# Kernel optimization log

Hardware: AMD Instinct MI355X
Metric: run time of the kernel (lower is better)

The kernel has to match this reference:

```python
import jax, jax.numpy as jnp
import numpy as np
import math

B, N, DMODEL, H = 8, 1024, 256, 8
HEAD_DIM = DMODEL // H


def setup_inputs() -> dict:
    key = jax.random.key(0)
    ks = jax.random.split(key, 8)
    x = jax.random.normal(ks[0], (B, N, DMODEL), dtype=jnp.float32)
    # symmetric-ish nonnegative pairwise distances
    adj = jax.random.uniform(ks[1], (B, N, N), dtype=jnp.float32) * 10.0
    mask = jax.random.uniform(ks[2], (B, N)) < 0.9  # bool, mostly valid nodes
    W_qkv = jax.random.normal(ks[3], (DMODEL, 3 * DMODEL), dtype=jnp.float32) / math.sqrt(DMODEL)
    b_qkv = jax.random.normal(ks[4], (3 * DMODEL,), dtype=jnp.float32) * 0.01
    shifts = jnp.arange(1.0, H + 1.0, dtype=jnp.float32)  # initial_shifts
    widths = jnp.ones((H,), dtype=jnp.float32)            # initial_widths
    # self_loop_W = 1/head_dim + U(0,1), non-trainable
    self_loop_w = 1.0 / HEAD_DIM + jax.random.uniform(ks[5], (H,), dtype=jnp.float32)
    return {"x": x, "adj": adj, "mask": mask, "W_qkv": W_qkv, "b_qkv": b_qkv,
            "shifts": shifts, "widths": widths, "self_loop_w": self_loop_w}


def reference(x, adj, mask, W_qkv, b_qkv, shifts, widths, self_loop_w):
    b, n, _ = x.shape
    h = shifts.shape[0]
    d = W_qkv.shape[1] // (3 * h)
    qkv = (x @ W_qkv + b_qkv).reshape(b, n, 3, h, d)
    qkv = jnp.transpose(qkv, (2, 0, 3, 1, 4))  # [3, B, H, N, D]
    Q, K, V = qkv[0], qkv[1], qkv[2]
    scores = jnp.einsum('bhnd,bhmd->bhnm', Q, K) / jnp.sqrt(jnp.float32(d))
    # Gaussian moire focus on adjacency distances, per head
    sh = shifts.reshape(1, h, 1, 1)
    w = jnp.maximum(widths, 0.5).reshape(1, h, 1, 1)
    moire = jnp.exp(-((adj[:, None, :, :] - sh) ** 2) / w)
    adjusted = scores + jnp.log(jnp.maximum(moire, 1e-6))
    eye = jnp.eye(n, dtype=adjusted.dtype)  # [N, N]
    adjusted = adjusted + eye * self_loop_w.reshape(1, h, 1, 1)
    mask2d = (mask[:, :, None] & mask[:, None, :])[:, None, :, :]  # [B,1,N,N]
    adjusted = jnp.where(mask2d, adjusted, jnp.float32(-1000000.0))
    attn = jax.nn.softmax(adjusted, axis=-1)
    out = jnp.einsum('bhnm,bhmd->bhnd', attn, V)
    return jnp.transpose(out, (0, 2, 1, 3)).reshape(b, n, h * d)
```

## Files before the change

kernel.cpp:

```cpp
#include <hip/hip_runtime.h>

#define BB 8
#define NN 1024
#define DM 256
#define HH 8
#define HD 32
#define TC 768

typedef __bf16 bf16x8 __attribute__((ext_vector_type(8)));
typedef __bf16 bf16x4 __attribute__((ext_vector_type(4)));
typedef float  f32x4  __attribute__((ext_vector_type(4)));

__global__ __launch_bounds__(256) void precast(
    const float* __restrict__ x, const float* __restrict__ W,
    __bf16* __restrict__ xb, __bf16* __restrict__ Wt)
{
  const int tid = threadIdx.x;
  const int bid = blockIdx.x;
  if (bid < 48) {
    __shared__ __bf16 T[64][65];
    const int ct = bid % 12, kt = bid / 12;
    const int c0 = ct * 64, k0 = kt * 64;
    #pragma unroll
    for (int i = 0; i < 16; ++i) {
      int e = tid + i * 256, kk = e >> 6, cc = e & 63;
      T[cc][kk] = (__bf16)W[(size_t)(k0 + kk) * TC + c0 + cc];
    }
    __syncthreads();
    #pragma unroll
    for (int i = 0; i < 16; ++i) {
      int e = tid + i * 256, cc = e >> 6, kk = e & 63;
      Wt[(size_t)(c0 + cc) * DM + k0 + kk] = T[cc][kk];
    }
  } else {
    const size_t e = (size_t)(bid - 48) * 256 + tid;
    const float4 v = ((const float4*)x)[e];
    bf16x4 o;
    o[0] = (__bf16)v.x; o[1] = (__bf16)v.y;
    o[2] = (__bf16)v.z; o[3] = (__bf16)v.w;
    ((bf16x4*)xb)[e] = o;
  }
}

__global__ __launch_bounds__(256, 4) void qkv_gemm(
    const __bf16* __restrict__ xb, const __bf16* __restrict__ Wt,
    const float* __restrict__ bias, __bf16* __restrict__ Qb,
    __bf16* __restrict__ Kb, __bf16* __restrict__ Vt)
{
  __shared__ __align__(16) char U[18432];
  __bf16* As = (__bf16*)U;
  __bf16* Bs = (__bf16*)(U + 10240);

  const int tid  = threadIdx.x;
  const int w    = tid >> 6, lane = tid & 63;
  const int n16  = lane & 15, quad = lane >> 4;
  const int m0   = blockIdx.y * 128, c0 = blockIdx.x * 64;
  const int bb   = m0 >> 10, n0 = m0 & 1023;

  const int arow = tid >> 1, ahalf = tid & 1;
  const int bc   = tid & 63, bkh = tid >> 6;

  f32x4 acc[2][4] = {};

  for (int k0 = 0; k0 < DM; k0 += 32) {
    {
      const __bf16* xa = &xb[(size_t)(m0 + arow) * DM + k0 + ahalf * 16];
      *(bf16x8*)&As[arow*40 + ahalf*16]     = *(const bf16x8*)&xa[0];
      *(bf16x8*)&As[arow*40 + ahalf*16 + 8] = *(const bf16x8*)&xa[8];
    }
    {
      *(bf16x8*)&Bs[bc*40 + bkh*8] =
          *(const bf16x8*)&Wt[(size_t)(c0 + bc) * DM + k0 + bkh*8];
    }
    __syncthreads();
    bf16x8 af0 = *(const bf16x8*)&As[(w*32 + n16)*40 + quad*8];
    bf16x8 af1 = *(const bf16x8*)&As[(w*32 + 16 + n16)*40 + quad*8];
    #pragma unroll
    for (int cb = 0; cb < 4; ++cb) {
      bf16x8 bf = *(const bf16x8*)&Bs[(cb*16 + n16)*40 + quad*8];
      acc[0][cb] = __builtin_amdgcn_mfma_f32_16x16x32_bf16(af0, bf, acc[0][cb], 0, 0, 0);
      acc[1][cb] = __builtin_amdgcn_mfma_f32_16x16x32_bf16(af1, bf, acc[1][cb], 0, 0, 0);
    }
    __syncthreads();
  }

  float bv[4];
  #pragma unroll
  for (int cb = 0; cb < 4; ++cb) bv[cb] = bias[c0 + cb*16 + n16];

  if (c0 < 512) {
    __bf16* Ct = (__bf16*)U;
    #pragma unroll
    for (int cb = 0; cb < 4; ++cb)
      #pragma unroll
      for (int mb = 0; mb < 2; ++mb)
        #pragma unroll
        for (int r = 0; r < 4; ++r)
          Ct[(w*32 + mb*16 + quad*4 + r)*72 + cb*16 + n16] =
              (__bf16)(acc[mb][cb][r] + bv[cb]);
    __syncthreads();
    const int chunk = tid & 3, hh = (tid >> 2) & 1, rbase = tid >> 3;
    const int c_head = c0 + hh*32;
    const int h = (c_head >> 5) & 7;
    __bf16* base = (c_head >> 8) ? Kb : Qb;
    #pragma unroll
    for (int it = 0; it < 4; ++it) {
      int rl = rbase + it*32;
      bf16x8 v = *(const bf16x8*)&Ct[rl*72 + hh*32 + chunk*8];
      *(bf16x8*)&base[((size_t)((bb*HH + h)*NN + n0 + rl))*HD + chunk*8] = v;
    }
  } else {
    __bf16* CtT = (__bf16*)U;
    #pragma unroll
    for (int cb = 0; cb < 4; ++cb)
      #pragma unroll
      for (int mb = 0; mb < 2; ++mb) {
        bf16x4 t;
        #pragma unroll
        for (int r = 0; r < 4; ++r) t[r] = (__bf16)(acc[mb][cb][r] + bv[cb]);
        *(bf16x4*)&CtT[(cb*16 + n16)*136 + w*32 + mb*16 + quad*4] = t;
      }
    __syncthreads();
    const int col = tid >> 2, sg = tid & 3;
    const int c = c0 + col;
    const int h = (c >> 5) & 7, dd = c & 31;
    __bf16* dst = &Vt[((size_t)((bb*HH + h)*HD + dd))*NN + n0 + sg*32];
    const __bf16* srcp = &CtT[col*136 + sg*32];
    #pragma unroll
    for (int q2 = 0; q2 < 4; ++q2)
      *(bf16x8*)&dst[q2*8] = *(const bf16x8*)&srcp[q2*8];
  }
}

template <int NJT, bool SPLIT>
__global__ __launch_bounds__(256, 4) void attn_kernel(
    const __bf16* __restrict__ Q, const __bf16* __restrict__ K,
    const __bf16* __restrict__ Vt, const float* __restrict__ adj,
    const int* __restrict__ mask, const float* __restrict__ shifts,
    const float* __restrict__ widths, const float* __restrict__ slw,
    float* __restrict__ out, float* __restrict__ Opart,
    float* __restrict__ lpart)
{
  __shared__ __align__(16) char U[9216];
  __bf16 (*Qs)[40] = (__bf16(*)[40])U;
  __bf16 (*Ps)[72] = (__bf16(*)[72])U;
  __shared__ __align__(16) __bf16 Ks[2][64][40];
  __shared__ __align__(16) __bf16 Vts[2][32][72];

  const int tid  = threadIdx.x;
  const int w    = tid >> 6, lane = tid & 63;
  const int n16  = lane & 15, quad = lane >> 4;
  const int bh   = blockIdx.x >> 4, qt = blockIdx.x & 15;
  const int part = blockIdx.y;
  const int b    = bh >> 3, h = bh & 7;
  const int q0   = qt * 64;
  const int jbase = part * NJT * 64;

  const float L2E   = 1.4426950408889634f;
  const float sh    = shifts[h];
  const float ninvw = -L2E / fmaxf(widths[h], 0.5f);
  const float slv   = slw[h] * L2E;
  const float scl   = 0.17677669529663687f * L2E;
  const float LGEPS = -19.931568569324174f;
  const float MASKV = -28.0f;

  const int srow = tid >> 2, sseg = tid & 3;
  const int vd   = tid >> 3, vsg  = tid & 7;

  {
    const __bf16* Qg = Q + (size_t)(bh*NN + q0)*HD;
    *(bf16x8*)&Qs[srow][sseg*8] = *(const bf16x8*)&Qg[srow*HD + sseg*8];
  }
  const __bf16* Kg = K + (size_t)bh*NN*HD;
  const __bf16* Vg = Vt + (size_t)bh*HD*NN;
  {
    *(bf16x8*)&Ks[0][srow][sseg*8] =
        *(const bf16x8*)&Kg[(jbase + srow)*HD + sseg*8];
    *(bf16x8*)&Vts[0][vd][vsg*8] =
        *(const bf16x8*)&Vg[(size_t)vd*NN + jbase + vsg*8];
  }
  int mq[4];
  #pragma unroll
  for (int r = 0; r < 4; ++r) mq[r] = mask[b*NN + q0 + w*16 + quad*4 + r];
  __syncthreads();
  const bf16x8 qf = *(const bf16x8*)&Qs[w*16 + n16][quad*8];
  __syncthreads();

  const f32x4 zero = {0.f, 0.f, 0.f, 0.f};
  float l_r[4] = {0.f, 0.f, 0.f, 0.f};
  f32x4 o0 = zero, o1 = zero;

  const float* adjRow = adj + ((size_t)(b*NN + q0 + w*16 + quad*4))*NN;
  const int*   mrow   = mask + b*NN;

  #pragma unroll 2
  for (int jtl = 0; jtl < NJT; ++jtl) {
    const int cur = jtl & 1;
    const int j0  = jbase + jtl * 64;

    bf16x8 kn, vn;
    if (jtl < NJT - 1) {
      kn = *(const bf16x8*)&Kg[(j0 + 64 + srow)*HD + sseg*8];
      vn = *(const bf16x8*)&Vg[(size_t)vd*NN + j0 + 64 + vsg*8];
    }

    int mj[4];
    #pragma unroll
    for (int cb = 0; cb < 4; ++cb) mj[cb] = mrow[j0 + cb*16 + n16];
    float av[4][4];
    #pragma unroll
    for (int r = 0; r < 4; ++r)
      #pragma unroll
      for (int cb = 0; cb < 4; ++cb)
        av[r][cb] = adjRow[(size_t)r*NN + j0 + cb*16 + n16];

    f32x4 s[4];
    #pragma unroll
    for (int cb = 0; cb < 4; ++cb) {
      bf16x8 kf = *(const bf16x8*)&Ks[cur][cb*16 + n16][quad*8];
      s[cb] = __builtin_amdgcn_mfma_f32_16x16x32_bf16(qf, kf, zero, 0, 0, 0);
    }

    const bool diagtile = ((part * NJT + jtl) == qt);
    #pragma unroll
    for (int r = 0; r < 4; ++r) {
      const int rowl = w*16 + quad*4 + r;
      #pragma unroll
      for (int cb = 0; cb < 4; ++cb) {
        float d   = av[r][cb] - sh;
        float mo  = fmaxf(d*d*ninvw, LGEPS);
        float val = fmaf(s[cb][r], scl, mo);
        if (diagtile && (cb*16 + n16 == rowl)) val += slv;
        bool ok = (mq[r] != 0) && (mj[cb] != 0);
        val = ok ? val : MASKV;
        float p = __builtin_amdgcn_exp2f(val);
        l_r[r] += p;
        Ps[rowl][cb*16 + n16] = (__bf16)p;
      }
    }

    bf16x8 a0  = *(const bf16x8*)&Ps[w*16 + n16][quad*8];
    bf16x8 a1  = *(const bf16x8*)&Ps[w*16 + n16][32 + quad*8];
    bf16x8 b00 = *(const bf16x8*)&Vts[cur][n16][quad*8];
    bf16x8 b01 = *(const bf16x8*)&Vts[cur][n16][32 + quad*8];
    bf16x8 b10 = *(const bf16x8*)&Vts[cur][16 + n16][quad*8];
    bf16x8 b11 = *(const bf16x8*)&Vts[cur][16 + n16][32 + quad*8];
    o0 = __builtin_amdgcn_mfma_f32_16x16x32_bf16(a0, b00, o0, 0, 0, 0);
    o0 = __builtin_amdgcn_mfma_f32_16x16x32_bf16(a1, b01, o0, 0, 0, 0);
    o1 = __builtin_amdgcn_mfma_f32_16x16x32_bf16(a0, b10, o1, 0, 0, 0);
    o1 = __builtin_amdgcn_mfma_f32_16x16x32_bf16(a1, b11, o1, 0, 0, 0);

    if (jtl < NJT - 1) {
      *(bf16x8*)&Ks[1 - cur][srow][sseg*8] = kn;
      *(bf16x8*)&Vts[1 - cur][vd][vsg*8]   = vn;
    }
    __syncthreads();
  }

  #pragma unroll
  for (int r = 0; r < 4; ++r) {
    float l = l_r[r];
    l += __shfl_xor(l, 1); l += __shfl_xor(l, 2);
    l += __shfl_xor(l, 4); l += __shfl_xor(l, 8);
    const int n = q0 + w*16 + quad*4 + r;
    if (SPLIT) {
      float* og = Opart + ((size_t)(part*BB*HH + bh)*NN + n)*HD;
      og[n16]      = o0[r];
      og[16 + n16] = o1[r];
      if (n16 == 0) lpart[(size_t)(part*BB*HH + bh)*NN + n] = l;
    } else {
      const float invl = 1.0f / l;
      float* og = out + ((size_t)(b*NN + n))*DM + h*HD;
      og[n16]      = o0[r] * invl;
      og[16 + n16] = o1[r] * invl;
    }
  }
}

__global__ __launch_bounds__(256) void combine_kernel(
    const float* __restrict__ Opart, const float* __restrict__ lpart,
    float* __restrict__ out)
{
  const size_t e = (size_t)blockIdx.x * 256 + threadIdx.x;
  const int c = (int)((e << 2) & 255);
  const int n = (int)((e >> 6) & 1023);
  const int b = (int)(e >> 16);
  const int h = c >> 5, d = c & 31;
  const size_t row = (size_t)(b*HH + h)*NN + n;
  const size_t i0  = row*HD + d;
  const size_t ps  = (size_t)BB*HH*NN*HD;
  const float4 a0 = *(const float4*)&Opart[i0];
  const float4 a1 = *(const float4*)&Opart[ps + i0];
  const float  l  = lpart[row] + lpart[(size_t)BB*HH*NN + row];
  const float invl = 1.0f / l;
  float4 o = {(a0.x + a1.x)*invl, (a0.y + a1.y)*invl,
              (a0.z + a1.z)*invl, (a0.w + a1.w)*invl};
  *(float4*)&out[((size_t)(b*NN + n))*DM + c] = o;
}

extern "C" void kernel_launch(void* const* d_in, const int* in_sizes, int n_in,
                              void* d_out, int out_size, void* d_ws, size_t ws_size,
                              hipStream_t stream) {
  const float* x      = (const float*)d_in[0];
  const float* adj    = (const float*)d_in[1];
  const int*   mask   = (const int*)d_in[2];
  const float* W      = (const float*)d_in[3];
  const float* bias   = (const float*)d_in[4];
  const float* shifts = (const float*)d_in[5];
  const float* widths = (const float*)d_in[6];
  const float* slwp   = (const float*)d_in[7];
  float* out = (float*)d_out;

  const size_t BHND = (size_t)BB*HH*NN*HD;
  const size_t WTN  = (size_t)TC*DM;
  __bf16* xbuf = (__bf16*)d_ws;
  __bf16* Wt   = xbuf + BHND;
  __bf16* Qb   = Wt + WTN;
  __bf16* Kb   = Qb + BHND;
  __bf16* Vt   = Kb + BHND;
  float*  Opart = (float*)(Vt + BHND);
  float*  lpart = Opart + 2*BHND;
  const size_t need = (4*BHND + WTN)*2 + 2*BHND*4 + 2*(size_t)BB*HH*NN*4;

  precast<<<dim3(48 + (int)(BHND/4/256)), 256, 0, stream>>>(x, W, xbuf, Wt);
  qkv_gemm<<<dim3(TC/64, (BB*NN)/128), 256, 0, stream>>>(xbuf, Wt, bias, Qb, Kb, Vt);

  if (ws_size >= need) {
    attn_kernel<8, true><<<dim3(BB*HH*16, 2), 256, 0, stream>>>(
        Qb, Kb, Vt, adj, mask, shifts, widths, slwp, out, Opart, lpart);
    combine_kernel<<<(int)(BHND/4/256), 256, 0, stream>>>(Opart, lpart, out);
  } else {
    attn_kernel<16, false><<<dim3(BB*HH*16, 1), 256, 0, stream>>>(
        Qb, Kb, Vt, adj, mask, shifts, widths, slwp, out, Opart, lpart);
  }
}
```

Measured before the change: 143.9 us.

## Drop split-K attention with combine pass; register-prefetch GEMM tiles

```diff
diff --git a/kernel.cpp b/kernel.cpp
--- a/kernel.cpp
+++ b/kernel.cpp
@@ -62,17 +62,22 @@
 
   f32x4 acc[2][4] = {};
 
+  const __bf16* xa_base = &xb[(size_t)(m0 + arow) * DM + ahalf * 16];
+  const __bf16* wb_base = &Wt[(size_t)(c0 + bc) * DM + bkh * 8];
+  bf16x8 ra0 = *(const bf16x8*)&xa_base[0];
+  bf16x8 ra1 = *(const bf16x8*)&xa_base[8];
+  bf16x8 rb  = *(const bf16x8*)&wb_base[0];
+
   for (int k0 = 0; k0 < DM; k0 += 32) {
-    {
-      const __bf16* xa = &xb[(size_t)(m0 + arow) * DM + k0 + ahalf * 16];
-      *(bf16x8*)&As[arow*40 + ahalf*16]     = *(const bf16x8*)&xa[0];
-      *(bf16x8*)&As[arow*40 + ahalf*16 + 8] = *(const bf16x8*)&xa[8];
-    }
-    {
-      *(bf16x8*)&Bs[bc*40 + bkh*8] =
-          *(const bf16x8*)&Wt[(size_t)(c0 + bc) * DM + k0 + bkh*8];
-    }
-    __syncthreads();
+    *(bf16x8*)&As[arow*40 + ahalf*16]     = ra0;
+    *(bf16x8*)&As[arow*40 + ahalf*16 + 8] = ra1;
+    *(bf16x8*)&Bs[bc*40 + bkh*8]          = rb;
+    __syncthreads();
+    if (k0 + 32 < DM) {
+      ra0 = *(const bf16x8*)&xa_base[k0 + 32];
+      ra1 = *(const bf16x8*)&xa_base[k0 + 40];
+      rb  = *(const bf16x8*)&wb_base[k0 + 32];
+    }
     bf16x8 af0 = *(const bf16x8*)&As[(w*32 + n16)*40 + quad*8];
     bf16x8 af1 = *(const bf16x8*)&As[(w*32 + 16 + n16)*40 + quad*8];
     #pragma unroll
@@ -132,14 +137,12 @@
   }
 }
 
-template <int NJT, bool SPLIT>
 __global__ __launch_bounds__(256, 4) void attn_kernel(
     const __bf16* __restrict__ Q, const __bf16* __restrict__ K,
     const __bf16* __restrict__ Vt, const float* __restrict__ adj,
     const int* __restrict__ mask, const float* __restrict__ shifts,
     const float* __restrict__ widths, const float* __restrict__ slw,
-    float* __restrict__ out, float* __restrict__ Opart,
-    float* __restrict__ lpart)
+    float* __restrict__ out)
 {
   __shared__ __align__(16) char U[9216];
   __bf16 (*Qs)[40] = (__bf16(*)[40])U;
@@ -151,10 +154,8 @@
   const int w    = tid >> 6, lane = tid & 63;
   const int n16  = lane & 15, quad = lane >> 4;
   const int bh   = blockIdx.x >> 4, qt = blockIdx.x & 15;
-  const int part = blockIdx.y;
   const int b    = bh >> 3, h = bh & 7;
   const int q0   = qt * 64;
-  const int jbase = part * NJT * 64;
 
   const float L2E   = 1.4426950408889634f;
   const float sh    = shifts[h];
@@ -174,10 +175,8 @@
   const __bf16* Kg = K + (size_t)bh*NN*HD;
   const __bf16* Vg = Vt + (size_t)bh*HD*NN;
   {
-    *(bf16x8*)&Ks[0][srow][sseg*8] =
-        *(const bf16x8*)&Kg[(jbase + srow)*HD + sseg*8];
-    *(bf16x8*)&Vts[0][vd][vsg*8] =
-        *(const bf16x8*)&Vg[(size_t)vd*NN + jbase + vsg*8];
+    *(bf16x8*)&Ks[0][srow][sseg*8] = *(const bf16x8*)&Kg[srow*HD + sseg*8];
+    *(bf16x8*)&Vts[0][vd][vsg*8]   = *(const bf16x8*)&Vg[(size_t)vd*NN + vsg*8];
   }
   int mq[4];
   #pragma unroll
@@ -194,12 +193,12 @@
   const int*   mrow   = mask + b*NN;
 
   #pragma unroll 2
-  for (int jtl = 0; jtl < NJT; ++jtl) {
+  for (int jtl = 0; jtl < 16; ++jtl) {
     const int cur = jtl & 1;
-    const int j0  = jbase + jtl * 64;
+    const int j0  = jtl * 64;
 
     bf16x8 kn, vn;
-    if (jtl < NJT - 1) {
+    if (jtl < 15) {
       kn = *(const bf16x8*)&Kg[(j0 + 64 + srow)*HD + sseg*8];
       vn = *(const bf16x8*)&Vg[(size_t)vd*NN + j0 + 64 + vsg*8];
     }
@@ -221,7 +220,7 @@
       s[cb] = __builtin_amdgcn_mfma_f32_16x16x32_bf16(qf, kf, zero, 0, 0, 0);
     }
 
-    const bool diagtile = ((part * NJT + jtl) == qt);
+    const bool diagtile = (jtl == qt);
     #pragma unroll
     for (int r = 0; r < 4; ++r) {
       const int rowl = w*16 + quad*4 + r;
@@ -250,7 +249,7 @@
     o1 = __builtin_amdgcn_mfma_f32_16x16x32_bf16(a0, b10, o1, 0, 0, 0);
     o1 = __builtin_amdgcn_mfma_f32_16x16x32_bf16(a1, b11, o1, 0, 0, 0);
 
-    if (jtl < NJT - 1) {
+    if (jtl < 15) {
       *(bf16x8*)&Ks[1 - cur][srow][sseg*8] = kn;
       *(bf16x8*)&Vts[1 - cur][vd][vsg*8]   = vn;
     }
@@ -262,40 +261,12 @@
     float l = l_r[r];
     l += __shfl_xor(l, 1); l += __shfl_xor(l, 2);
     l += __shfl_xor(l, 4); l += __shfl_xor(l, 8);
+    const float invl = 1.0f / l;
     const int n = q0 + w*16 + quad*4 + r;
-    if (SPLIT) {
-      float* og = Opart + ((size_t)(part*BB*HH + bh)*NN + n)*HD;
-      og[n16]      = o0[r];
-      og[16 + n16] = o1[r];
-      if (n16 == 0) lpart[(size_t)(part*BB*HH + bh)*NN + n] = l;
-    } else {
-      const float invl = 1.0f / l;
-      float* og = out + ((size_t)(b*NN + n))*DM + h*HD;
-      og[n16]      = o0[r] * invl;
-      og[16 + n16] = o1[r] * invl;
-    }
-  }
-}
-
-__global__ __launch_bounds__(256) void combine_kernel(
-    const float* __restrict__ Opart, const float* __restrict__ lpart,
-    float* __restrict__ out)
-{
-  const size_t e = (size_t)blockIdx.x * 256 + threadIdx.x;
-  const int c = (int)((e << 2) & 255);
-  const int n = (int)((e >> 6) & 1023);
-  const int b = (int)(e >> 16);
-  const int h = c >> 5, d = c & 31;
-  const size_t row = (size_t)(b*HH + h)*NN + n;
-  const size_t i0  = row*HD + d;
-  const size_t ps  = (size_t)BB*HH*NN*HD;
-  const float4 a0 = *(const float4*)&Opart[i0];
-  const float4 a1 = *(const float4*)&Opart[ps + i0];
-  const float  l  = lpart[row] + lpart[(size_t)BB*HH*NN + row];
-  const float invl = 1.0f / l;
-  float4 o = {(a0.x + a1.x)*invl, (a0.y + a1.y)*invl,
-              (a0.z + a1.z)*invl, (a0.w + a1.w)*invl};
-  *(float4*)&out[((size_t)(b*NN + n))*DM + c] = o;
+    float* og = out + ((size_t)(b*NN + n))*DM + h*HD;
+    og[n16]      = o0[r] * invl;
+    og[16 + n16] = o1[r] * invl;
+  }
 }
 
 extern "C" void kernel_launch(void* const* d_in, const int* in_sizes, int n_in,
@@ -318,19 +289,9 @@
   __bf16* Qb   = Wt + WTN;
   __bf16* Kb   = Qb + BHND;
   __bf16* Vt   = Kb + BHND;
-  float*  Opart = (float*)(Vt + BHND);
-  float*  lpart = Opart + 2*BHND;
-  const size_t need = (4*BHND + WTN)*2 + 2*BHND*4 + 2*(size_t)BB*HH*NN*4;
 
   precast<<<dim3(48 + (int)(BHND/4/256)), 256, 0, stream>>>(x, W, xbuf, Wt);
   qkv_gemm<<<dim3(TC/64, (BB*NN)/128), 256, 0, stream>>>(xbuf, Wt, bias, Qb, Kb, Vt);
-
-  if (ws_size >= need) {
-    attn_kernel<8, true><<<dim3(BB*HH*16, 2), 256, 0, stream>>>(
-        Qb, Kb, Vt, adj, mask, shifts, widths, slwp, out, Opart, lpart);
-    combine_kernel<<<(int)(BHND/4/256), 256, 0, stream>>>(Opart, lpart, out);
-  } else {
-    attn_kernel<16, false><<<dim3(BB*HH*16, 1), 256, 0, stream>>>(
-        Qb, Kb, Vt, adj, mask, shifts, widths, slwp, out, Opart, lpart);
-  }
-}
+  attn_kernel<<<dim3(BB*HH*16), 256, 0, stream>>>(Qb, Kb, Vt, adj, mask,
+                                                  shifts, widths, slwp, out);
+}
```

After: 137.5 us. -4.5%, faster.
